# Kernel optimization log

Hardware: AMD Instinct MI355X
Metric: run time of the kernel (lower is better)

The kernel has to match this reference:

```python
import jax, jax.numpy as jnp
import numpy as np

N_NODES = 100000
N_EDGES = 1250000
N_PAIRS = 200000
IN_DIM = 128
HID = 64
N_LAYERS = 3


def setup_inputs() -> dict:
    key = jax.random.key(0)
    ks = jax.random.split(key, 16)
    x = jax.random.normal(ks[0], (N_NODES, IN_DIM), dtype=jnp.float32)
    edge_index = jax.random.randint(ks[1], (2, N_EDGES), 0, N_NODES, dtype=jnp.int64)
    pair_index = jax.random.randint(ks[2], (N_PAIRS, 2), 0, N_NODES, dtype=jnp.int64)
    s_in = 1.0 / np.sqrt(IN_DIM)
    s_h = 1.0 / np.sqrt(HID)
    s_2h = 1.0 / np.sqrt(2 * HID)
    enc_W = jax.random.uniform(ks[3], (IN_DIM, HID), jnp.float32, -s_in, s_in)
    enc_b = jax.random.uniform(ks[4], (HID,), jnp.float32, -s_in, s_in)
    # SAGEConv params per layer: lin_l (neighbors, with bias), lin_r (root, no bias)
    Wl = jax.random.uniform(ks[5], (N_LAYERS, HID, HID), jnp.float32, -s_h, s_h)
    bl = jax.random.uniform(ks[6], (N_LAYERS, HID), jnp.float32, -s_h, s_h)
    Wr = jax.random.uniform(ks[7], (N_LAYERS, HID, HID), jnp.float32, -s_h, s_h)
    # predictor MLP: Linear(2h -> h), ReLU, Linear(h -> 1)
    W1 = jax.random.uniform(ks[8], (2 * HID, HID), jnp.float32, -s_2h, s_2h)
    b1 = jax.random.uniform(ks[9], (HID,), jnp.float32, -s_2h, s_2h)
    W2 = jax.random.uniform(ks[10], (HID, 1), jnp.float32, -s_h, s_h)
    b2 = jax.random.uniform(ks[11], (1,), jnp.float32, -s_h, s_h)
    return {"x": x, "edge_index": edge_index, "pair_index": pair_index,
            "enc_W": enc_W, "enc_b": enc_b, "Wl": Wl, "bl": bl, "Wr": Wr,
            "W1": W1, "b1": b1, "W2": W2, "b2": b2}


def reference(x, edge_index, pair_index, enc_W, enc_b, Wl, bl, Wr, W1, b1, W2, b2):
    src, dst = edge_index[0], edge_index[1]
    n = x.shape[0]
    # neighbor counts for mean aggregation (empty neighborhoods -> 0, matching PyG)
    deg = jax.ops.segment_sum(jnp.ones((src.shape[0],), x.dtype), dst, num_segments=n)
    inv_deg = jnp.where(deg > 0, 1.0 / jnp.maximum(deg, 1.0), 0.0)[:, None]  # [N,1]
    # node encoder: Linear + ReLU
    h = jax.nn.relu(x @ enc_W + enc_b)  # [N, HID]
    for i in range(Wl.shape[0]):
        # scatter-mean of source features onto destinations
        agg = jax.ops.segment_sum(h[src], dst, num_segments=n) * inv_deg  # [N, HID]
        h = jax.nn.relu(agg @ Wl[i] + bl[i] + h @ Wr[i])
        # dropout is identity in eval mode
    z = jnp.concatenate([h[pair_index[:, 0]], h[pair_index[:, 1]]], axis=1)  # [P, 2*HID]
    out = (jax.nn.relu(z @ W1 + b1) @ W2 + b2)[:, 0]  # [P]
    return out
```

## Files before the change

kernel.cpp:

```cpp
#include <hip/hip_runtime.h>
#include <hip/hip_fp16.h>
#include <cstdint>
#include <cstddef>

#define N_NODES_C 100000
#define N_EDGES_C 1250000
#define N_PAIRS_C 200000
#define IN_DIM_C 128
#define HID_C 64

#define NB_S 256
#define BSH 9
#define NPB 512
#define NBKT 196
#define SEG_CAP 8192

typedef _Float16 f16x8 __attribute__((ext_vector_type(8)));
typedef float f32x4 __attribute__((ext_vector_type(4)));


#define SCAN_TPB 256
#define SCAN_IPT 4
#define SCAN_ELEMS 1024

__global__ void k_scan_partial(const int* __restrict__ in, int* __restrict__ outp,
                               int* __restrict__ blocksums, int n) {
    __shared__ int sd[SCAN_TPB];
    int tid = threadIdx.x;
    int base = blockIdx.x * SCAN_ELEMS + tid * SCAN_IPT;
    int v[SCAN_IPT]; int s = 0;
    for (int k = 0; k < SCAN_IPT; k++) { int idx = base + k; v[k] = (idx < n) ? in[idx] : 0; s += v[k]; }
    sd[tid] = s;
    __syncthreads();
    for (int off = 1; off < SCAN_TPB; off <<= 1) {
        int t = (tid >= off) ? sd[tid - off] : 0;
        __syncthreads();
        sd[tid] += t;
        __syncthreads();
    }
    int excl = sd[tid] - s;
    for (int k = 0; k < SCAN_IPT; k++) { int idx = base + k; if (idx < n) outp[idx] = excl; excl += v[k]; }
    if (tid == SCAN_TPB - 1) blocksums[blockIdx.x] = sd[tid];
}

__global__ void k_scan_blocks(int* __restrict__ bs, int nb) {
    __shared__ int sd[128];
    int t = threadIdx.x;
    int v = (t < nb) ? bs[t] : 0;
    sd[t] = v;
    __syncthreads();
    for (int off = 1; off < 128; off <<= 1) {
        int u = (t >= off) ? sd[t - off] : 0;
        __syncthreads();
        sd[t] += u;
        __syncthreads();
    }
    if (t < nb) bs[t] = sd[t] - v;
}

__global__ void k_scan_addg(int* __restrict__ arr, const int* __restrict__ bs, int n) {
    int i = blockIdx.x * blockDim.x + threadIdx.x;
    if (i < n) arr[i] += bs[i >> 10];
}


__global__ __launch_bounds__(256) void k_hist(const int* __restrict__ dst,
                                              int* __restrict__ histT, int e) {
    __shared__ int lh[NBKT];
    int tid = threadIdx.x, k = blockIdx.x;
    if (tid < NBKT) lh[tid] = 0;
    __syncthreads();
    int chunk = (e + NB_S - 1) / NB_S;
    int i0 = k * chunk, i1 = min(i0 + chunk, e);
    for (int i = i0 + tid; i < i1; i += 256) atomicAdd(&lh[dst[i] >> BSH], 1);
    __syncthreads();
    if (tid < NBKT) histT[tid * NB_S + k] = lh[tid];
}

__global__ __launch_bounds__(256) void k_scatter(const int* __restrict__ edges,
                                                 const int* __restrict__ offs,
                                                 int2* __restrict__ staging, int e) {
    __shared__ int cur[NBKT];
    int tid = threadIdx.x, k = blockIdx.x;
    if (tid < NBKT) cur[tid] = offs[tid * NB_S + k];
    __syncthreads();
    int chunk = (e + NB_S - 1) / NB_S;
    int i0 = k * chunk, i1 = min(i0 + chunk, e);
    for (int i = i0 + tid; i < i1; i += 256) {
        int s = edges[i];
        int d = edges[e + i];
        int p = atomicAdd(&cur[d >> BSH], 1);
        staging[p] = make_int2(s, d);
    }
}

__global__ __launch_bounds__(256) void k_bucket_fill(const int2* __restrict__ staging,
        const int* __restrict__ offs, int* __restrict__ rowptr,
        float* __restrict__ invd, int* __restrict__ adj, int n, int e) {
    __shared__ int ldeg[NPB];
    __shared__ int lrow[NPB];
    __shared__ int ps[256];
    __shared__ int lseg[SEG_CAP];
    int tid = threadIdx.x, b = blockIdx.x;
    int n0 = b << BSH;
    int nn = min(NPB, n - n0);
    int segBeg = offs[b * NB_S];
    int segEnd = (b == NBKT - 1) ? e : offs[(b + 1) * NB_S];

    ldeg[tid] = 0; ldeg[tid + 256] = 0;
    __syncthreads();
    for (int i = segBeg + tid; i < segEnd; i += 256)
        atomicAdd(&ldeg[staging[i].y - n0], 1);
    __syncthreads();

    int a0 = ldeg[2 * tid], a1 = ldeg[2 * tid + 1];
    int s = a0 + a1;
    ps[tid] = s;
    __syncthreads();
    for (int off = 1; off < 256; off <<= 1) {
        int t = (tid >= off) ? ps[tid - off] : 0;
        __syncthreads();
        ps[tid] += t;
        __syncthreads();
    }
    int excl = ps[tid] - s;
    lrow[2 * tid] = excl;
    lrow[2 * tid + 1] = excl + a0;
    __syncthreads();

    for (int j = tid; j < nn; j += 256) {
        rowptr[n0 + j] = segBeg + lrow[j];
        int d = ldeg[j];
        invd[n0 + j] = (d > 0) ? (1.0f / (float)d) : 0.0f;
    }
    if (b == NBKT - 1 && tid == 0) rowptr[n] = e;
    __syncthreads();

    for (int i = segBeg + tid; i < segEnd; i += 256) {
        int2 ed = staging[i];
        int p = atomicAdd(&lrow[ed.y - n0], 1);
        if (p < SEG_CAP) lseg[p] = ed.x;
        else adj[segBeg + p] = ed.x;
    }
    __syncthreads();

    int m = segEnd - segBeg; if (m > SEG_CAP) m = SEG_CAP;
    for (int p = tid; p < m; p += 256) adj[segBeg + p] = lseg[p];
}


__global__ __launch_bounds__(256) void k_aggregate(const int* __restrict__ rowptr,
        const int* __restrict__ adj, const float* __restrict__ invd,
        const __half* __restrict__ hin16, __half* __restrict__ agg16, int n) {
    int wid = threadIdx.x >> 6, lane = threadIdx.x & 63;
    int node0 = (blockIdx.x * 4 + wid) * 8;
    if (node0 >= n) return;
    const int q = lane >> 3;
    const int c8 = (lane & 7) * 8;
    int node = node0 + q;
    bool valid = node < n;
    int nodec = valid ? node : n - 1;
    int beg = rowptr[nodec], end = rowptr[nodec + 1];
    float a0 = 0.f, a1 = 0.f, a2 = 0.f, a3 = 0.f;
    float a4 = 0.f, a5 = 0.f, a6 = 0.f, a7 = 0.f;
    for (int e = beg; e < end; e += 8) {
        int idx[8];
        #pragma unroll
        for (int j = 0; j < 8; ++j) {
            int ee = e + j;
            idx[j] = adj[ee < end ? ee : end - 1];
        }
        float4 raw[8];
        #pragma unroll
        for (int j = 0; j < 8; ++j)
            raw[j] = *(const float4*)&hin16[(size_t)idx[j] * HID_C + c8];
        #pragma unroll
        for (int j = 0; j < 8; ++j) {
            union { float4 f; __half2 h[4]; } u;
            u.f = raw[j];
            float2 f0 = __half22float2(u.h[0]);
            float2 f1 = __half22float2(u.h[1]);
            float2 f2 = __half22float2(u.h[2]);
            float2 f3 = __half22float2(u.h[3]);
            bool in = (e + j < end);
            a0 += in ? f0.x : 0.f;  a1 += in ? f0.y : 0.f;
            a2 += in ? f1.x : 0.f;  a3 += in ? f1.y : 0.f;
            a4 += in ? f2.x : 0.f;  a5 += in ? f2.y : 0.f;
            a6 += in ? f3.x : 0.f;  a7 += in ? f3.y : 0.f;
        }
    }
    if (valid) {
        float s = invd[node];
        union { float4 f; __half2 h[4]; } o;
        o.h[0] = __floats2half2_rn(a0 * s, a1 * s);
        o.h[1] = __floats2half2_rn(a2 * s, a3 * s);
        o.h[2] = __floats2half2_rn(a4 * s, a5 * s);
        o.h[3] = __floats2half2_rn(a6 * s, a7 * s);
        *(float4*)&agg16[(size_t)node * HID_C + c8] = o.f;
    }
}


__device__ __forceinline__ float4 ld4(const float* p) { return *(const float4*)p; }


template<int SRC>
__global__ __launch_bounds__(256, 2) void k_mm(
    const float* __restrict__ A1f,
    const __half* __restrict__ A1h, const __half* __restrict__ A2h,
    const float* __restrict__ Ws1, const float* __restrict__ Ws2,
    const float* __restrict__ bias,
    __half* __restrict__ out16, int nrows)
{
    __shared__ __half Ah[128 * 128];
    __shared__ __half Bt[64 * 128];
    const int t = threadIdx.x;
    const int g0 = blockIdx.x * 128;

    #pragma unroll
    for (int p = 0; p < 8; ++p) {
        int li = p * 256 + t;
        int r = li >> 4;
        int o = li & 15;
        int g = g0 + r; if (g > nrows - 1) g = nrows - 1;
        f16x8 v;
        if (SRC == 0) {
            const float* src = A1f + (size_t)g * 128 + o * 8;
            float4 f0 = ld4(src), f1 = ld4(src + 4);
            v[0] = (_Float16)f0.x; v[1] = (_Float16)f0.y;
            v[2] = (_Float16)f0.z; v[3] = (_Float16)f0.w;
            v[4] = (_Float16)f1.x; v[5] = (_Float16)f1.y;
            v[6] = (_Float16)f1.z; v[7] = (_Float16)f1.w;
        } else {
            const __half* src = (o < 8) ? (A1h + (size_t)g * 64 + o * 8)
                                        : (A2h + (size_t)g * 64 + (o - 8) * 8);
            v = *(const f16x8*)src;
        }
        *(f16x8*)&Ah[r * 128 + (o ^ (r & 15)) * 8] = v;
    }
    #pragma unroll
    for (int p = 0; p < 32; ++p) {
        int li = p * 256 + t;
        int c = li & 63;
        int k = li >> 6;
        float wv;
        if (SRC == 0) wv = Ws1[k * 64 + c];
        else          wv = (k < 64) ? Ws1[k * 64 + c] : Ws2[(k - 64) * 64 + c];
        Bt[c * 128 + (((k >> 3) ^ (c & 15)) * 8) + (k & 7)] = __float2half(wv);
    }
    __syncthreads();

    const int lane = t & 63;
    const int wid = t >> 6;
    const int R = wid * 32;
    const int lr = lane & 15;
    const int lk = lane >> 4;

    f32x4 acc[2][4];
    #pragma unroll
    for (int fr = 0; fr < 2; ++fr)
        #pragma unroll
        for (int fc = 0; fc < 4; ++fc)
            acc[fr][fc] = (f32x4){0.f, 0.f, 0.f, 0.f};

    #pragma unroll
    for (int ks = 0; ks < 4; ++ks) {
        int o = ks * 4 + lk;
        f16x8 af0, af1;
        {
            int r0 = R + lr;
            int r1 = R + 16 + lr;
            af0 = *(const f16x8*)&Ah[r0 * 128 + (o ^ (r0 & 15)) * 8];
            af1 = *(const f16x8*)&Ah[r1 * 128 + (o ^ (r1 & 15)) * 8];
        }
        #pragma unroll
        for (int fc = 0; fc < 4; ++fc) {
            int c = fc * 16 + lr;
            f16x8 bf = *(const f16x8*)&Bt[c * 128 + (o ^ (c & 15)) * 8];
            acc[0][fc] = __builtin_amdgcn_mfma_f32_16x16x32_f16(af0, bf, acc[0][fc], 0, 0, 0);
            acc[1][fc] = __builtin_amdgcn_mfma_f32_16x16x32_f16(af1, bf, acc[1][fc], 0, 0, 0);
        }
    }

    float bv[4];
    #pragma unroll
    for (int fc = 0; fc < 4; ++fc) bv[fc] = bias[fc * 16 + lr];
    #pragma unroll
    for (int fr = 0; fr < 2; ++fr) {
        #pragma unroll
        for (int j = 0; j < 4; ++j) {
            int gr = g0 + R + fr * 16 + lk * 4 + j;
            if (gr < nrows) {
                #pragma unroll
                for (int fc = 0; fc < 4; ++fc) {
                    int col = fc * 16 + lr;
                    float v = fmaxf(acc[fr][fc][j] + bv[fc], 0.f);
                    out16[(size_t)gr * 64 + col] = __float2half(v);
                }
            }
        }
    }
}


__global__ __launch_bounds__(256, 2) void k_mm_uv(
    const __half* __restrict__ A1h, const __half* __restrict__ A2h,
    const float* __restrict__ Ws1, const float* __restrict__ Ws2,
    const float* __restrict__ bias, const float* __restrict__ W1p,
    __half* __restrict__ U16, __half* __restrict__ V16, int nrows)
{
    __shared__ __half Ah[128 * 128];
    __shared__ __half Bt[64 * 128];
    const int t = threadIdx.x;
    const int g0 = blockIdx.x * 128;

    #pragma unroll
    for (int p = 0; p < 8; ++p) {
        int li = p * 256 + t;
        int r = li >> 4;
        int o = li & 15;
        int g = g0 + r; if (g > nrows - 1) g = nrows - 1;
        const __half* src = (o < 8) ? (A1h + (size_t)g * 64 + o * 8)
                                    : (A2h + (size_t)g * 64 + (o - 8) * 8);
        f16x8 v = *(const f16x8*)src;
        *(f16x8*)&Ah[r * 128 + (o ^ (r & 15)) * 8] = v;
    }
    #pragma unroll
    for (int p = 0; p < 32; ++p) {
        int li = p * 256 + t;
        int c = li & 63;
        int k = li >> 6;
        float wv = (k < 64) ? Ws1[k * 64 + c] : Ws2[(k - 64) * 64 + c];
        Bt[c * 128 + (((k >> 3) ^ (c & 15)) * 8) + (k & 7)] = __float2half(wv);
    }
    __syncthreads();

    const int lane = t & 63;
    const int wid = t >> 6;
    const int R = wid * 32;
    const int lr = lane & 15;
    const int lk = lane >> 4;

    f32x4 acc[2][4];
    #pragma unroll
    for (int fr = 0; fr < 2; ++fr)
        #pragma unroll
        for (int fc = 0; fc < 4; ++fc)
            acc[fr][fc] = (f32x4){0.f, 0.f, 0.f, 0.f};

    #pragma unroll
    for (int ks = 0; ks < 4; ++ks) {
        int o = ks * 4 + lk;
        int r0 = R + lr, r1 = R + 16 + lr;
        f16x8 af0 = *(const f16x8*)&Ah[r0 * 128 + (o ^ (r0 & 15)) * 8];
        f16x8 af1 = *(const f16x8*)&Ah[r1 * 128 + (o ^ (r1 & 15)) * 8];
        #pragma unroll
        for (int fc = 0; fc < 4; ++fc) {
            int c = fc * 16 + lr;
            f16x8 bf = *(const f16x8*)&Bt[c * 128 + (o ^ (c & 15)) * 8];
            acc[0][fc] = __builtin_amdgcn_mfma_f32_16x16x32_f16(af0, bf, acc[0][fc], 0, 0, 0);
            acc[1][fc] = __builtin_amdgcn_mfma_f32_16x16x32_f16(af1, bf, acc[1][fc], 0, 0, 0);
        }
    }

    float bv[4];
    #pragma unroll
    for (int fc = 0; fc < 4; ++fc) bv[fc] = bias[fc * 16 + lr];

    __syncthreads();

    #pragma unroll
    for (int fr = 0; fr < 2; ++fr) {
        #pragma unroll
        for (int j = 0; j < 4; ++j) {
            int lrow = R + fr * 16 + lk * 4 + j;
            #pragma unroll
            for (int fc = 0; fc < 4; ++fc) {
                int col = fc * 16 + lr;
                float v = fmaxf(acc[fr][fc][j] + bv[fc], 0.f);
                int o = col >> 3;
                Ah[lrow * 64 + ((o ^ (lrow & 7)) * 8) + (col & 7)] = __float2half(v);
            }
        }
    }
    #pragma unroll
    for (int p = 0; p < 32; ++p) {
        int li = p * 256 + t;
        int c = li & 127;
        int k = li >> 7;
        float wv = (c < 64) ? W1p[k * 64 + c] : W1p[(64 + k) * 64 + (c - 64)];
        Bt[c * 64 + (((k >> 3) ^ (c & 7)) * 8) + (k & 7)] = __float2half(wv);
    }
    __syncthreads();

    f32x4 acc2[2][8];
    #pragma unroll
    for (int fr = 0; fr < 2; ++fr)
        #pragma unroll
        for (int fc = 0; fc < 8; ++fc)
            acc2[fr][fc] = (f32x4){0.f, 0.f, 0.f, 0.f};

    #pragma unroll
    for (int ks = 0; ks < 2; ++ks) {
        int o = ks * 4 + lk;
        int r0 = R + lr, r1 = R + 16 + lr;
        f16x8 af0 = *(const f16x8*)&Ah[r0 * 64 + (o ^ (r0 & 7)) * 8];
        f16x8 af1 = *(const f16x8*)&Ah[r1 * 64 + (o ^ (r1 & 7)) * 8];
        #pragma unroll
        for (int fc = 0; fc < 8; ++fc) {
            int c = fc * 16 + lr;
            f16x8 bf = *(const f16x8*)&Bt[c * 64 + (o ^ (c & 7)) * 8];
            acc2[0][fc] = __builtin_amdgcn_mfma_f32_16x16x32_f16(af0, bf, acc2[0][fc], 0, 0, 0);
            acc2[1][fc] = __builtin_amdgcn_mfma_f32_16x16x32_f16(af1, bf, acc2[1][fc], 0, 0, 0);
        }
    }

    #pragma unroll
    for (int fr = 0; fr < 2; ++fr) {
        #pragma unroll
        for (int j = 0; j < 4; ++j) {
            int gr = g0 + R + fr * 16 + lk * 4 + j;
            if (gr < nrows) {
                #pragma unroll
                for (int fc = 0; fc < 8; ++fc) {
                    int col = fc * 16 + lr;
                    __half v = __float2half(acc2[fr][fc][j]);
                    if (col < 64) U16[(size_t)gr * 64 + col] = v;
                    else          V16[(size_t)gr * 64 + (col - 64)] = v;
                }
            }
        }
    }
}

__global__ __launch_bounds__(256) void k_pred(
    const __half* __restrict__ U16, const __half* __restrict__ V16,
    const int* __restrict__ pidx, const float* __restrict__ b1,
    const float* __restrict__ W2, const float* __restrict__ b2,
    float* __restrict__ outp, int np)
{
    const int t = threadIdx.x;
    const int lg = t & 15;
    const int p = blockIdx.x * 16 + (t >> 4);
    float4 bv = ld4(b1 + lg * 4);
    float4 wv = ld4(W2 + lg * 4);
    if (p >= np) return;
    int2 ab = ((const int2*)pidx)[p];
    float2 ur = *(const float2*)&U16[(size_t)ab.x * 64 + lg * 4];
    float2 vr = *(const float2*)&V16[(size_t)ab.y * 64 + lg * 4];
    union { float f; __half2 h; } u0, u1, v0, v1;
    u0.f = ur.x; u1.f = ur.y; v0.f = vr.x; v1.f = vr.y;
    float2 ua = __half22float2(u0.h), ub = __half22float2(u1.h);
    float2 va = __half22float2(v0.h), vb = __half22float2(v1.h);
    float zx = fmaxf(ua.x + va.x + bv.x, 0.f);
    float zy = fmaxf(ua.y + va.y + bv.y, 0.f);
    float zz = fmaxf(ub.x + vb.x + bv.z, 0.f);
    float zw = fmaxf(ub.y + vb.y + bv.w, 0.f);
    float s = zx * wv.x + zy * wv.y + zz * wv.z + zw * wv.w;
    s += __shfl_down(s, 8, 16);
    s += __shfl_down(s, 4, 16);
    s += __shfl_down(s, 2, 16);
    s += __shfl_down(s, 1, 16);
    if (lg == 0) outp[p] = s + b2[0];
}


extern "C" void kernel_launch(void* const* d_in, const int* in_sizes, int n_in,
                              void* d_out, int out_size, void* d_ws, size_t ws_size,
                              hipStream_t stream) {
    const float* x    = (const float*)d_in[0];
    const int*   edges= (const int*)d_in[1];
    const int*   pair = (const int*)d_in[2];
    const float* encW = (const float*)d_in[3];
    const float* encb = (const float*)d_in[4];
    const float* Wl   = (const float*)d_in[5];
    const float* bl   = (const float*)d_in[6];
    const float* Wr   = (const float*)d_in[7];
    const float* W1   = (const float*)d_in[8];
    const float* b1   = (const float*)d_in[9];
    const float* W2   = (const float*)d_in[10];
    const float* b2   = (const float*)d_in[11];
    float* out = (float*)d_out;

    const int N = N_NODES_C, E = N_EDGES_C, P = N_PAIRS_C;
    const int* dst = edges + E;
    const int M = NBKT * NB_S;

    char* w = (char*)d_ws;
    auto alloc = [&](size_t bytes) { char* p = w; w += (bytes + 255) & ~(size_t)255; return p; };
    int*   rowptr = (int*)alloc((size_t)(N + 1) * 4);
    int*   histT  = (int*)alloc((size_t)M * 4);
    int*   offs   = (int*)alloc((size_t)M * 4);
    int*   bsums  = (int*)alloc(128 * 4);
    float* invd   = (float*)alloc((size_t)N * 4);
    int*   adj    = (int*)alloc((size_t)E * 4);
    int2*  staging= (int2*)alloc((size_t)E * 8);
    __half* h16a  = (__half*)alloc((size_t)N * HID_C * 2);
    __half* h16b  = (__half*)alloc((size_t)N * HID_C * 2);
    __half* agg16 = (__half*)alloc((size_t)N * HID_C * 2);
    __half* U16   = (__half*)alloc((size_t)N * HID_C * 2);
    __half* V16   = (__half*)alloc((size_t)N * HID_C * 2);

    int nscan = (M + SCAN_ELEMS - 1) / SCAN_ELEMS;

    hipLaunchKernelGGL(k_hist, dim3(NB_S), dim3(256), 0, stream, dst, histT, E);
    hipLaunchKernelGGL(k_scan_partial, dim3(nscan), dim3(SCAN_TPB), 0, stream, histT, offs, bsums, M);
    hipLaunchKernelGGL(k_scan_blocks, dim3(1), dim3(128), 0, stream, bsums, nscan);
    hipLaunchKernelGGL(k_scan_addg, dim3((M + 255) / 256), dim3(256), 0, stream, offs, bsums, M);
    hipLaunchKernelGGL(k_scatter, dim3(NB_S), dim3(256), 0, stream, edges, offs, staging, E);
    hipLaunchKernelGGL(k_bucket_fill, dim3(NBKT), dim3(256), 0, stream, staging, offs, rowptr, invd, adj, N, E);

    const int NB128 = (N + 127) / 128;

    k_mm<0><<<dim3(NB128), dim3(256), 0, stream>>>(
        x, nullptr, nullptr, encW, nullptr, encb, h16a, N);

    __half* h16c = h16a; __half* h16n = h16b;
    for (int l = 0; l < 2; l++) {
        hipLaunchKernelGGL(k_aggregate, dim3((N + 31) / 32), dim3(256), 0, stream,
                           rowptr, adj, invd, h16c, agg16, N);
        k_mm<1><<<dim3(NB128), dim3(256), 0, stream>>>(
            nullptr, agg16, h16c, Wl + (size_t)l * 64 * 64, Wr + (size_t)l * 64 * 64,
            bl + (size_t)l * 64, h16n, N);
        __half* t16 = h16c; h16c = h16n; h16n = t16;
    }

    hipLaunchKernelGGL(k_aggregate, dim3((N + 31) / 32), dim3(256), 0, stream,
                       rowptr, adj, invd, h16c, agg16, N);
    hipLaunchKernelGGL(k_mm_uv, dim3(NB128), dim3(256), 0, stream,
                       agg16, h16c, Wl + (size_t)2 * 64 * 64, Wr + (size_t)2 * 64 * 64,
                       bl + (size_t)2 * 64, W1, U16, V16, N);

    hipLaunchKernelGGL(k_pred, dim3((P + 15) / 16), dim3(256), 0, stream,
                       U16, V16, pair, b1, W2, b2, out, P);
}
```

Before: 296.9 us.

## Fuse CSR build kernels into one cooperative kernel with grid syncs

```diff
diff --git a/kernel.cpp b/kernel.cpp
--- a/kernel.cpp
+++ b/kernel.cpp
@@ -1,7 +1,10 @@
 #include <hip/hip_runtime.h>
 #include <hip/hip_fp16.h>
+#include <hip/hip_cooperative_groups.h>
 #include <cstdint>
 #include <cstddef>
+
+namespace cg = cooperative_groups;
 
 #define N_NODES_C 100000
 #define N_EDGES_C 1250000
@@ -15,137 +18,145 @@
 #define NBKT 196
 #define SEG_CAP 8192
 
-typedef _Float16 f16x8 __attribute__((ext_vector_type(8)));
-typedef float f32x4 __attribute__((ext_vector_type(4)));
-
-
 #define SCAN_TPB 256
 #define SCAN_IPT 4
 #define SCAN_ELEMS 1024
 
-__global__ void k_scan_partial(const int* __restrict__ in, int* __restrict__ outp,
-                               int* __restrict__ blocksums, int n) {
-    __shared__ int sd[SCAN_TPB];
-    int tid = threadIdx.x;
-    int base = blockIdx.x * SCAN_ELEMS + tid * SCAN_IPT;
-    int v[SCAN_IPT]; int s = 0;
-    for (int k = 0; k < SCAN_IPT; k++) { int idx = base + k; v[k] = (idx < n) ? in[idx] : 0; s += v[k]; }
-    sd[tid] = s;
-    __syncthreads();
-    for (int off = 1; off < SCAN_TPB; off <<= 1) {
-        int t = (tid >= off) ? sd[tid - off] : 0;
-        __syncthreads();
-        sd[tid] += t;
-        __syncthreads();
-    }
-    int excl = sd[tid] - s;
-    for (int k = 0; k < SCAN_IPT; k++) { int idx = base + k; if (idx < n) outp[idx] = excl; excl += v[k]; }
-    if (tid == SCAN_TPB - 1) blocksums[blockIdx.x] = sd[tid];
-}
-
-__global__ void k_scan_blocks(int* __restrict__ bs, int nb) {
-    __shared__ int sd[128];
-    int t = threadIdx.x;
-    int v = (t < nb) ? bs[t] : 0;
-    sd[t] = v;
-    __syncthreads();
-    for (int off = 1; off < 128; off <<= 1) {
-        int u = (t >= off) ? sd[t - off] : 0;
-        __syncthreads();
-        sd[t] += u;
-        __syncthreads();
-    }
-    if (t < nb) bs[t] = sd[t] - v;
-}
-
-__global__ void k_scan_addg(int* __restrict__ arr, const int* __restrict__ bs, int n) {
-    int i = blockIdx.x * blockDim.x + threadIdx.x;
-    if (i < n) arr[i] += bs[i >> 10];
-}
-
-
-__global__ __launch_bounds__(256) void k_hist(const int* __restrict__ dst,
-                                              int* __restrict__ histT, int e) {
-    __shared__ int lh[NBKT];
-    int tid = threadIdx.x, k = blockIdx.x;
-    if (tid < NBKT) lh[tid] = 0;
-    __syncthreads();
-    int chunk = (e + NB_S - 1) / NB_S;
-    int i0 = k * chunk, i1 = min(i0 + chunk, e);
-    for (int i = i0 + tid; i < i1; i += 256) atomicAdd(&lh[dst[i] >> BSH], 1);
-    __syncthreads();
-    if (tid < NBKT) histT[tid * NB_S + k] = lh[tid];
-}
-
-__global__ __launch_bounds__(256) void k_scatter(const int* __restrict__ edges,
-                                                 const int* __restrict__ offs,
-                                                 int2* __restrict__ staging, int e) {
-    __shared__ int cur[NBKT];
-    int tid = threadIdx.x, k = blockIdx.x;
-    if (tid < NBKT) cur[tid] = offs[tid * NB_S + k];
-    __syncthreads();
-    int chunk = (e + NB_S - 1) / NB_S;
-    int i0 = k * chunk, i1 = min(i0 + chunk, e);
-    for (int i = i0 + tid; i < i1; i += 256) {
-        int s = edges[i];
-        int d = edges[e + i];
-        int p = atomicAdd(&cur[d >> BSH], 1);
-        staging[p] = make_int2(s, d);
-    }
-}
-
-__global__ __launch_bounds__(256) void k_bucket_fill(const int2* __restrict__ staging,
-        const int* __restrict__ offs, int* __restrict__ rowptr,
-        float* __restrict__ invd, int* __restrict__ adj, int n, int e) {
-    __shared__ int ldeg[NPB];
-    __shared__ int lrow[NPB];
-    __shared__ int ps[256];
-    __shared__ int lseg[SEG_CAP];
-    int tid = threadIdx.x, b = blockIdx.x;
-    int n0 = b << BSH;
-    int nn = min(NPB, n - n0);
-    int segBeg = offs[b * NB_S];
-    int segEnd = (b == NBKT - 1) ? e : offs[(b + 1) * NB_S];
-
-    ldeg[tid] = 0; ldeg[tid + 256] = 0;
-    __syncthreads();
-    for (int i = segBeg + tid; i < segEnd; i += 256)
-        atomicAdd(&ldeg[staging[i].y - n0], 1);
-    __syncthreads();
-
-    int a0 = ldeg[2 * tid], a1 = ldeg[2 * tid + 1];
-    int s = a0 + a1;
-    ps[tid] = s;
-    __syncthreads();
-    for (int off = 1; off < 256; off <<= 1) {
-        int t = (tid >= off) ? ps[tid - off] : 0;
-        __syncthreads();
-        ps[tid] += t;
-        __syncthreads();
-    }
-    int excl = ps[tid] - s;
-    lrow[2 * tid] = excl;
-    lrow[2 * tid + 1] = excl + a0;
-    __syncthreads();
-
-    for (int j = tid; j < nn; j += 256) {
-        rowptr[n0 + j] = segBeg + lrow[j];
-        int d = ldeg[j];
-        invd[n0 + j] = (d > 0) ? (1.0f / (float)d) : 0.0f;
-    }
-    if (b == NBKT - 1 && tid == 0) rowptr[n] = e;
-    __syncthreads();
-
-    for (int i = segBeg + tid; i < segEnd; i += 256) {
-        int2 ed = staging[i];
-        int p = atomicAdd(&lrow[ed.y - n0], 1);
-        if (p < SEG_CAP) lseg[p] = ed.x;
-        else adj[segBeg + p] = ed.x;
-    }
-    __syncthreads();
-
-    int m = segEnd - segBeg; if (m > SEG_CAP) m = SEG_CAP;
-    for (int p = tid; p < m; p += 256) adj[segBeg + p] = lseg[p];
+typedef _Float16 f16x8 __attribute__((ext_vector_type(8)));
+typedef float f32x4 __attribute__((ext_vector_type(4)));
+
+
+__global__ __launch_bounds__(256) void k_build(
+    const int* __restrict__ edges, int* __restrict__ histT,
+    int* __restrict__ offs, int* __restrict__ bsums,
+    int2* __restrict__ staging, int* __restrict__ rowptr,
+    float* __restrict__ invd, int* __restrict__ adj)
+{
+    constexpr int E = N_EDGES_C;
+    constexpr int n = N_NODES_C;
+    constexpr int M = NBKT * NB_S;
+    constexpr int nscan = (M + SCAN_ELEMS - 1) / SCAN_ELEMS;
+    const int* dst = edges + E;
+    __shared__ int smem[2 * NPB + 256 + SEG_CAP];
+    const int tid = threadIdx.x;
+    const int blk = blockIdx.x;
+    cg::grid_group grid = cg::this_grid();
+
+    {
+        int* lh = smem;
+        if (tid < NBKT) lh[tid] = 0;
+        __syncthreads();
+        int chunk = (E + NB_S - 1) / NB_S;
+        int i0 = blk * chunk, i1 = min(i0 + chunk, E);
+        for (int i = i0 + tid; i < i1; i += 256) atomicAdd(&lh[dst[i] >> BSH], 1);
+        __syncthreads();
+        if (tid < NBKT) histT[tid * NB_S + blk] = lh[tid];
+    }
+    grid.sync();
+
+    if (blk < nscan) {
+        int* sd = smem;
+        int base = blk * SCAN_ELEMS + tid * SCAN_IPT;
+        int v[SCAN_IPT]; int s = 0;
+        for (int k = 0; k < SCAN_IPT; k++) { int idx = base + k; v[k] = (idx < M) ? histT[idx] : 0; s += v[k]; }
+        sd[tid] = s;
+        __syncthreads();
+        for (int off = 1; off < SCAN_TPB; off <<= 1) {
+            int t2 = (tid >= off) ? sd[tid - off] : 0;
+            __syncthreads();
+            sd[tid] += t2;
+            __syncthreads();
+        }
+        int excl = sd[tid] - s;
+        for (int k = 0; k < SCAN_IPT; k++) { int idx = base + k; if (idx < M) offs[idx] = excl; excl += v[k]; }
+        if (tid == SCAN_TPB - 1) bsums[blk] = sd[tid];
+    }
+    grid.sync();
+
+    if (blk == 0) {
+        int* sd = smem;
+        int v = (tid < nscan) ? bsums[tid] : 0;
+        sd[tid] = v;
+        __syncthreads();
+        for (int off = 1; off < 256; off <<= 1) {
+            int u = (tid >= off) ? sd[tid - off] : 0;
+            __syncthreads();
+            sd[tid] += u;
+            __syncthreads();
+        }
+        if (tid < nscan) bsums[tid] = sd[tid] - v;
+    }
+    grid.sync();
+
+    for (int i = blk * 256 + tid; i < M; i += NB_S * 256)
+        offs[i] += bsums[i >> 10];
+    grid.sync();
+
+    {
+        int* cur = smem;
+        if (tid < NBKT) cur[tid] = offs[tid * NB_S + blk];
+        __syncthreads();
+        int chunk = (E + NB_S - 1) / NB_S;
+        int i0 = blk * chunk, i1 = min(i0 + chunk, E);
+        for (int i = i0 + tid; i < i1; i += 256) {
+            int s = edges[i];
+            int d = edges[E + i];
+            int p = atomicAdd(&cur[d >> BSH], 1);
+            staging[p] = make_int2(s, d);
+        }
+    }
+    grid.sync();
+
+    if (blk < NBKT) {
+        int* ldeg = smem;
+        int* lrow = smem + NPB;
+        int* ps   = smem + 2 * NPB;
+        int* lseg = smem + 2 * NPB + 256;
+        int n0 = blk << BSH;
+        int nn = min(NPB, n - n0);
+        int segBeg = offs[blk * NB_S];
+        int segEnd = (blk == NBKT - 1) ? E : offs[(blk + 1) * NB_S];
+
+        ldeg[tid] = 0; ldeg[tid + 256] = 0;
+        __syncthreads();
+        for (int i = segBeg + tid; i < segEnd; i += 256)
+            atomicAdd(&ldeg[staging[i].y - n0], 1);
+        __syncthreads();
+
+        int a0 = ldeg[2 * tid], a1 = ldeg[2 * tid + 1];
+        int s = a0 + a1;
+        ps[tid] = s;
+        __syncthreads();
+        for (int off = 1; off < 256; off <<= 1) {
+            int t2 = (tid >= off) ? ps[tid - off] : 0;
+            __syncthreads();
+            ps[tid] += t2;
+            __syncthreads();
+        }
+        int excl = ps[tid] - s;
+        lrow[2 * tid] = excl;
+        lrow[2 * tid + 1] = excl + a0;
+        __syncthreads();
+
+        for (int j = tid; j < nn; j += 256) {
+            rowptr[n0 + j] = segBeg + lrow[j];
+            int d = ldeg[j];
+            invd[n0 + j] = (d > 0) ? (1.0f / (float)d) : 0.0f;
+        }
+        if (blk == NBKT - 1 && tid == 0) rowptr[n] = E;
+        __syncthreads();
+
+        for (int i = segBeg + tid; i < segEnd; i += 256) {
+            int2 ed = staging[i];
+            int p = atomicAdd(&lrow[ed.y - n0], 1);
+            if (p < SEG_CAP) lseg[p] = ed.x;
+            else adj[segBeg + p] = ed.x;
+        }
+        __syncthreads();
+
+        int m = segEnd - segBeg; if (m > SEG_CAP) m = SEG_CAP;
+        for (int p = tid; p < m; p += 256) adj[segBeg + p] = lseg[p];
+    }
 }
 
 
@@ -483,7 +494,6 @@
     float* out = (float*)d_out;
 
     const int N = N_NODES_C, E = N_EDGES_C, P = N_PAIRS_C;
-    const int* dst = edges + E;
     const int M = NBKT * NB_S;
 
     char* w = (char*)d_ws;
@@ -501,14 +511,12 @@
     __half* U16   = (__half*)alloc((size_t)N * HID_C * 2);
     __half* V16   = (__half*)alloc((size_t)N * HID_C * 2);
 
-    int nscan = (M + SCAN_ELEMS - 1) / SCAN_ELEMS;
-
-    hipLaunchKernelGGL(k_hist, dim3(NB_S), dim3(256), 0, stream, dst, histT, E);
-    hipLaunchKernelGGL(k_scan_partial, dim3(nscan), dim3(SCAN_TPB), 0, stream, histT, offs, bsums, M);
-    hipLaunchKernelGGL(k_scan_blocks, dim3(1), dim3(128), 0, stream, bsums, nscan);
-    hipLaunchKernelGGL(k_scan_addg, dim3((M + 255) / 256), dim3(256), 0, stream, offs, bsums, M);
-    hipLaunchKernelGGL(k_scatter, dim3(NB_S), dim3(256), 0, stream, edges, offs, staging, E);
-    hipLaunchKernelGGL(k_bucket_fill, dim3(NBKT), dim3(256), 0, stream, staging, offs, rowptr, invd, adj, N, E);
+    {
+        void* args[] = { (void*)&edges, (void*)&histT, (void*)&offs, (void*)&bsums,
+                         (void*)&staging, (void*)&rowptr, (void*)&invd, (void*)&adj };
+        hipLaunchCooperativeKernel((const void*)k_build, dim3(NB_S), dim3(256),
+                                   args, 0, stream);
+    }
 
     const int NB128 = (N + 127) / 128;
 
```

Measured after the change: 463.8 us. +56.2%, slower.
